# Kernel optimization log

Measured on AMD Instinct MI355X. Metric: run time of the kernel, lower is better.

## Reference

```python
import jax, jax.numpy as jnp
import numpy as np

INPUT_DIM = 512
HIDDEN_DIM = 1024


def glorot_normal(key, shape):
    fan_in, fan_out = shape[0], shape[1]
    std = jnp.sqrt(2.0 / (fan_in + fan_out))
    return std * jax.random.normal(key, shape, dtype=jnp.float32)


def setup_inputs() -> dict:
    key = jax.random.key(0)
    k1, k2, k3 = jax.random.split(key, 3)
    b, t = 32, 1024
    H = HIDDEN_DIM + INPUT_DIM
    x_btd = jax.random.normal(k1, (b, t, INPUT_DIM), dtype=jnp.float32)
    input_paddings = jnp.zeros((b, t), dtype=jnp.float32)
    kernel = glorot_normal(k2, (H, 4 * HIDDEN_DIM))  # [H, 4h]
    bias = jnp.zeros((4 * HIDDEN_DIM,), dtype=jnp.float32)
    h_init = glorot_normal(k3, (1, HIDDEN_DIM))
    return {"x_btd": x_btd, "input_paddings": input_paddings,
            "kernel": kernel, "bias": bias, "h_init": h_init}


def lstm_step(carry, x_bd, kernel, bias):
    h_bh, c_bh = carry
    x_bH = jnp.concatenate([x_bd, h_bh], axis=-1)          # [b, d+h]
    gate_out = jnp.einsum('bH,Hh->bh', x_bH, kernel) + bias  # [b, 4h]
    f, i, o, g = jnp.split(gate_out, 4, axis=-1)
    c_new = jax.nn.sigmoid(f) * c_bh + jax.nn.sigmoid(i) * jnp.tanh(g)
    h_new = jax.nn.sigmoid(o) * jnp.tanh(c_new)
    return (h_new, c_new), h_new


def reference(x_btd, input_paddings, kernel, bias, h_init) -> jnp.ndarray:
    del input_paddings
    b = x_btd.shape[0]
    h0 = jnp.tile(h_init, (b, 1))                # [b, h]
    c0 = jnp.zeros((b, HIDDEN_DIM), dtype=x_btd.dtype)
    x_tbd = jnp.transpose(x_btd, (1, 0, 2))      # [t, b, d]

    def step(carry, x_bd):
        return lstm_step(carry, x_bd, kernel, bias)

    _, h_tbh = jax.lax.scan(step, (h0, c0), x_tbd)
    return jnp.transpose(h_tbh, (1, 0, 2))       # [b, t, h]
```

## Files before the change

kernel.cpp:

```cpp
#include <hip/hip_runtime.h>


#define T_STEPS 1024
#define BATCH   32
#define DIN     512
#define HID     1024
#define KTOT    1536
#define NBLK    128
#define WCOLS   32
#define WSTR    1544
#define REDSTR  33
#define REDW    (32*REDSTR)

#define LDS_W_BYTES   (WCOLS*WSTR*2)
#define LDS_RED_BYTES (4*REDW*4)
#define LDS_H_BYTES   (256*2)
#define LDS_TOTAL     (LDS_W_BYTES + LDS_RED_BYTES + LDS_H_BYTES)

typedef __attribute__((ext_vector_type(8))) short  short8;
typedef __attribute__((ext_vector_type(4))) float  floatx4;
typedef __attribute__((ext_vector_type(4))) unsigned short ushort4_;

__device__ __forceinline__ unsigned short f2bf(float f) {
    unsigned u = __builtin_bit_cast(unsigned, f);
    u += 0x7FFFu + ((u >> 16) & 1u);
    return (unsigned short)(u >> 16);
}
__device__ __forceinline__ float sigf(float x) { return 1.f / (1.f + __expf(-x)); }

__device__ __forceinline__ floatx4 coh_load16(const void* p) {
    floatx4 v;
    asm volatile("global_load_dwordx4 %0, %1, off sc1" : "=v"(v) : "v"(p));
    return v;
}
__device__ __forceinline__ int coh_load4(const void* p) {
    int v;
    asm volatile("global_load_dword %0, %1, off sc1\n\ts_waitcnt vmcnt(0)"
                 : "=v"(v) : "v"(p) : "memory");
    return v;
}
__device__ __forceinline__ void coh_store16(void* p, short8 v) {
    asm volatile("global_store_dwordx4 %0, %1, off sc1" :: "v"(p), "v"(v) : "memory");
}
__device__ __forceinline__ void coh_store4(void* p, int v) {
    asm volatile("global_store_dword %0, %1, off sc1" :: "v"(p), "v"(v) : "memory");
}
__device__ __forceinline__ void wait_vm0() {
    asm volatile("s_waitcnt vmcnt(0)" ::: "memory");
}

__global__ __launch_bounds__(256) void prep_wt(const float* __restrict__ kern,
                                               unsigned short* __restrict__ wt) {
    __shared__ unsigned short tile[64][72];
    const int c0 = (blockIdx.x & 63) * 64;
    const int k0 = (blockIdx.x >> 6) * 64;
    const int cl = threadIdx.x & 63;
    const int kg = threadIdx.x >> 6;
    #pragma unroll
    for (int i = 0; i < 16; ++i) {
        int kl = kg * 16 + i;
        tile[cl][kl] = f2bf(kern[(k0 + kl) * 4096 + c0 + cl]);
    }
    __syncthreads();
    #pragma unroll
    for (int i = 0; i < 16; ++i) {
        int cc = kg * 16 + i;
        wt[(size_t)(c0 + cc) * KTOT + k0 + cl] = tile[cc][cl];
    }
}

__global__ __launch_bounds__(256) void prep_x(const float* __restrict__ x,
                                              unsigned short* __restrict__ xT) {
    const int row = blockIdx.x * 2 + (threadIdx.x >> 7);
    const int l   = threadIdx.x & 127;
    const int b = row >> 10, t = row & 1023;
    float4 v = ((const float4*)(x + (size_t)row * DIN))[l];
    ushort4_ o;
    o.x = f2bf(v.x); o.y = f2bf(v.y); o.z = f2bf(v.z); o.w = f2bf(v.w);
    *(ushort4_*)(xT + ((size_t)t * BATCH + b) * DIN + l * 4) = o;
}

__global__ __launch_bounds__(256) void init_h(const float* __restrict__ h_init,
                                              unsigned short* __restrict__ hbuf,
                                              int* __restrict__ flags) {
    if (blockIdx.x == 32) {
        for (int i = threadIdx.x; i < NBLK * 4; i += 256) flags[i] = 0;
        return;
    }
    const int b = blockIdx.x;
    for (int u = threadIdx.x; u < HID; u += 256)
        hbuf[b * HID + u] = f2bf(h_init[u]);
}

__global__ __launch_bounds__(256, 1) void lstm_persist(
    const unsigned short* __restrict__ wt,
    const unsigned short* __restrict__ xT,
    unsigned short* __restrict__ hbuf,
    int* __restrict__ flags,
    const float* __restrict__ bias,
    float* __restrict__ out)
{
    extern __shared__ char smem[];
    unsigned short* ldsW = (unsigned short*)smem;
    float* red = (float*)(smem + LDS_W_BYTES);
    unsigned short* hLDS = (unsigned short*)(smem + LDS_W_BYTES + LDS_RED_BYTES);

    const int bk   = blockIdx.x;
    const int tid  = threadIdx.x;
    const int wave = tid >> 6;
    const int lane = tid & 63;
    const int lrow = lane & 15;
    const int kq   = lane >> 4;

    for (int cl = wave; cl < WCOLS; cl += 4) {
        const int gcol = (cl >> 3) * HID + bk * 8 + (cl & 7);
        const unsigned short* src = wt + (size_t)gcol * KTOT;
        unsigned short* dst = ldsW + cl * WSTR;
        for (int k = lane * 8; k < KTOT; k += 512)
            *(short8*)(dst + k) = *(const short8*)(src + k);
    }

    const int pb = tid >> 3;
    const int pu = tid & 7;
    float bias_r[4];
    #pragma unroll
    for (int g = 0; g < 4; ++g) bias_r[g] = bias[g * HID + bk * 8 + pu];
    float c_state = 0.f;

    const int* myflag = flags + (wave * 32 + (lane & 31)) * 4;
    __syncthreads();

    for (int t = 0; t < T_STEPS; ++t) {
        floatx4 zero = {0.f, 0.f, 0.f, 0.f};
        floatx4 acc[2][2];
        acc[0][0] = zero; acc[0][1] = zero; acc[1][0] = zero; acc[1][1] = zero;

        const unsigned short* xb = xT + (size_t)t * (BATCH * DIN);
        #pragma unroll
        for (int i = 0; i < 4; ++i) {
            const int kl = wave * 128 + i * 32 + kq * 8;
            short8 a0 = *(const short8*)(xb + lrow * DIN + kl);
            short8 a1 = *(const short8*)(xb + (lrow + 16) * DIN + kl);
            short8 b0 = *(const short8*)(ldsW + lrow * WSTR + kl);
            short8 b1 = *(const short8*)(ldsW + (lrow + 16) * WSTR + kl);
            acc[0][0] = __builtin_amdgcn_mfma_f32_16x16x32_bf16(a0, b0, acc[0][0], 0, 0, 0);
            acc[0][1] = __builtin_amdgcn_mfma_f32_16x16x32_bf16(a0, b1, acc[0][1], 0, 0, 0);
            acc[1][0] = __builtin_amdgcn_mfma_f32_16x16x32_bf16(a1, b0, acc[1][0], 0, 0, 0);
            acc[1][1] = __builtin_amdgcn_mfma_f32_16x16x32_bf16(a1, b1, acc[1][1], 0, 0, 0);
        }

        if (t > 0) {
            while (coh_load4(myflag) < t)
                __builtin_amdgcn_s_sleep(1);
        }

        const unsigned short* hb = hbuf + (size_t)(t & 1) * (BATCH * HID);
        floatx4 ha[8][2];
        #pragma unroll
        for (int i = 0; i < 8; ++i) {
            const int kh = wave * 256 + i * 32 + kq * 8;
            ha[i][0] = coh_load16(hb + lrow * HID + kh);
            ha[i][1] = coh_load16(hb + (lrow + 16) * HID + kh);
        }
        wait_vm0();
        #pragma unroll
        for (int i = 0; i < 8; ++i) {
            const int kw = 512 + wave * 256 + i * 32 + kq * 8;
            short8 a0 = __builtin_bit_cast(short8, ha[i][0]);
            short8 a1 = __builtin_bit_cast(short8, ha[i][1]);
            short8 b0 = *(const short8*)(ldsW + lrow * WSTR + kw);
            short8 b1 = *(const short8*)(ldsW + (lrow + 16) * WSTR + kw);
            acc[0][0] = __builtin_amdgcn_mfma_f32_16x16x32_bf16(a0, b0, acc[0][0], 0, 0, 0);
            acc[0][1] = __builtin_amdgcn_mfma_f32_16x16x32_bf16(a0, b1, acc[0][1], 0, 0, 0);
            acc[1][0] = __builtin_amdgcn_mfma_f32_16x16x32_bf16(a1, b0, acc[1][0], 0, 0, 0);
            acc[1][1] = __builtin_amdgcn_mfma_f32_16x16x32_bf16(a1, b1, acc[1][1], 0, 0, 0);
        }

        #pragma unroll
        for (int mt = 0; mt < 2; ++mt)
            #pragma unroll
            for (int nt = 0; nt < 2; ++nt)
                #pragma unroll
                for (int r = 0; r < 4; ++r) {
                    const int row = mt * 16 + kq * 4 + r;
                    const int col = nt * 16 + lrow;
                    red[wave * REDW + row * REDSTR + col] = acc[mt][nt][r];
                }
        __syncthreads();

        float gv[4];
        #pragma unroll
        for (int g = 0; g < 4; ++g) {
            const int col = g * 8 + pu;
            float s = bias_r[g];
            #pragma unroll
            for (int w = 0; w < 4; ++w) s += red[w * REDW + pb * REDSTR + col];
            gv[g] = s;
        }
        const float fg = sigf(gv[0]);
        const float ig = sigf(gv[1]);
        const float og = sigf(gv[2]);
        const float gg = tanhf(gv[3]);
        c_state = fg * c_state + ig * gg;
        const float hn = og * tanhf(c_state);

        out[(size_t)pb * (T_STEPS * HID) + (size_t)t * HID + bk * 8 + pu] = hn;
        hLDS[tid] = f2bf(hn);
        __syncthreads();

        if (wave == 0) {
            if (lane < 32) {
                short8 v = *(const short8*)(hLDS + lane * 8);
                unsigned short* hp = hbuf + (size_t)((t + 1) & 1) * (BATCH * HID)
                                          + lane * HID + bk * 8;
                coh_store16(hp, v);
            }
            wait_vm0();
            if (lane == 0)
                coh_store4(flags + bk * 4, t + 1);
        }
    }
}

extern "C" void kernel_launch(void* const* d_in, const int* in_sizes, int n_in,
                              void* d_out, int out_size, void* d_ws, size_t ws_size,
                              hipStream_t stream) {
    (void)in_sizes; (void)n_in; (void)out_size;
    const float* x      = (const float*)d_in[0];
    const float* kern   = (const float*)d_in[2];
    const float* bias   = (const float*)d_in[3];
    const float* h_init = (const float*)d_in[4];
    float* out = (float*)d_out;

    char* ws = (char*)d_ws;
    unsigned short* wt    = (unsigned short*)(ws);
    unsigned short* xT    = (unsigned short*)(ws + 12582912);
    unsigned short* hbuf  = (unsigned short*)(ws + 12582912 + 33554432);
    int*            flags = (int*)(ws + 12582912 + 33554432 + 131072);
    (void)ws_size;

    hipFuncSetAttribute((const void*)lstm_persist,
                        hipFuncAttributeMaxDynamicSharedMemorySize, LDS_TOTAL);

    prep_wt<<<dim3(64 * 24), dim3(256), 0, stream>>>(kern, wt);
    prep_x<<<dim3(BATCH * T_STEPS / 2), dim3(256), 0, stream>>>(x, xT);
    init_h<<<dim3(33), dim3(256), 0, stream>>>(h_init, hbuf, flags);

    void* args[] = { &wt, &xT, &hbuf, &flags, &bias, &out };
    hipLaunchCooperativeKernel((const void*)lstm_persist, dim3(NBLK), dim3(256),
                               args, LDS_TOTAL, stream);
}
```

Before: 4.970 ms.

## Split persistent LSTM block into x-projection and recurrent-h wave groups

Doubles the block to 512 threads. Four waves compute the input projection for the next step, and the other four poll flags and compute the recurrent h contribution, so the x GEMM leaves the critical path. The h buffer is reorganised into per-producer contiguous 256-element chunks, and flags are padded to separate 64-byte lines. A fast exp-based tanh replaces tanhf, and the reduction buffer grows to 8 slots. The risks are more LDS and register pressure, a changed barrier structure, and extra __syncthreads per step.

```diff
diff --git a/kernel.cpp b/kernel.cpp
--- a/kernel.cpp
+++ b/kernel.cpp
@@ -11,9 +11,11 @@
 #define WSTR    1544
 #define REDSTR  33
 #define REDW    (32*REDSTR)
+#define NSLOT   8
+#define FLAGSTR 16
 
 #define LDS_W_BYTES   (WCOLS*WSTR*2)
-#define LDS_RED_BYTES (4*REDW*4)
+#define LDS_RED_BYTES (NSLOT*REDW*4)
 #define LDS_H_BYTES   (256*2)
 #define LDS_TOTAL     (LDS_W_BYTES + LDS_RED_BYTES + LDS_H_BYTES)
 
@@ -27,6 +29,10 @@
     return (unsigned short)(u >> 16);
 }
 __device__ __forceinline__ float sigf(float x) { return 1.f / (1.f + __expf(-x)); }
+__device__ __forceinline__ float tanh_fast(float x) {
+    float e = __expf(2.f * x);
+    return 1.f - 2.f / (e + 1.f);
+}
 
 __device__ __forceinline__ floatx4 coh_load16(const void* p) {
     floatx4 v;
@@ -84,15 +90,19 @@
                                               unsigned short* __restrict__ hbuf,
                                               int* __restrict__ flags) {
     if (blockIdx.x == 32) {
-        for (int i = threadIdx.x; i < NBLK * 4; i += 256) flags[i] = 0;
+        for (int i = threadIdx.x; i < NBLK * FLAGSTR; i += 256) flags[i] = 0;
         return;
     }
-    const int b = blockIdx.x;
-    for (int u = threadIdx.x; u < HID; u += 256)
-        hbuf[b * HID + u] = f2bf(h_init[u]);
-}
-
-__global__ __launch_bounds__(256, 1) void lstm_persist(
+    const int p0 = blockIdx.x * 4;
+    const int u = threadIdx.x & 7;
+    #pragma unroll
+    for (int j = 0; j < 4; ++j) {
+        const int p = p0 + j;
+        hbuf[p * 256 + threadIdx.x] = f2bf(h_init[p * 8 + u]);
+    }
+}
+
+__global__ __launch_bounds__(512, 2) void lstm_persist(
     const unsigned short* __restrict__ wt,
     const unsigned short* __restrict__ xT,
     unsigned short* __restrict__ hbuf,
@@ -111,8 +121,10 @@
     const int lane = tid & 63;
     const int lrow = lane & 15;
     const int kq   = lane >> 4;
-
-    for (int cl = wave; cl < WCOLS; cl += 4) {
+    const bool isG = wave < 4;
+    const int  sl  = wave & 3;
+
+    for (int cl = wave; cl < WCOLS; cl += 8) {
         const int gcol = (cl >> 3) * HID + bk * 8 + (cl & 7);
         const unsigned short* src = wt + (size_t)gcol * KTOT;
         unsigned short* dst = ldsW + cl * WSTR;
@@ -123,102 +135,167 @@
     const int pb = tid >> 3;
     const int pu = tid & 7;
     float bias_r[4];
-    #pragma unroll
-    for (int g = 0; g < 4; ++g) bias_r[g] = bias[g * HID + bk * 8 + pu];
     float c_state = 0.f;
-
-    const int* myflag = flags + (wave * 32 + (lane & 31)) * 4;
+    if (tid < 256) {
+        #pragma unroll
+        for (int g = 0; g < 4; ++g) bias_r[g] = bias[g * HID + bk * 8 + pu];
+    }
+
+    const int* myflag = flags + (sl * 32 + (lane & 31)) * FLAGSTR;
     __syncthreads();
 
-    for (int t = 0; t < T_STEPS; ++t) {
+    {
         floatx4 zero = {0.f, 0.f, 0.f, 0.f};
         floatx4 acc[2][2];
         acc[0][0] = zero; acc[0][1] = zero; acc[1][0] = zero; acc[1][1] = zero;
-
-        const unsigned short* xb = xT + (size_t)t * (BATCH * DIN);
-        #pragma unroll
-        for (int i = 0; i < 4; ++i) {
-            const int kl = wave * 128 + i * 32 + kq * 8;
-            short8 a0 = *(const short8*)(xb + lrow * DIN + kl);
-            short8 a1 = *(const short8*)(xb + (lrow + 16) * DIN + kl);
-            short8 b0 = *(const short8*)(ldsW + lrow * WSTR + kl);
-            short8 b1 = *(const short8*)(ldsW + (lrow + 16) * WSTR + kl);
-            acc[0][0] = __builtin_amdgcn_mfma_f32_16x16x32_bf16(a0, b0, acc[0][0], 0, 0, 0);
-            acc[0][1] = __builtin_amdgcn_mfma_f32_16x16x32_bf16(a0, b1, acc[0][1], 0, 0, 0);
-            acc[1][0] = __builtin_amdgcn_mfma_f32_16x16x32_bf16(a1, b0, acc[1][0], 0, 0, 0);
-            acc[1][1] = __builtin_amdgcn_mfma_f32_16x16x32_bf16(a1, b1, acc[1][1], 0, 0, 0);
+        if (isG) {
+            const unsigned short* xb = xT;
+            #pragma unroll
+            for (int i = 0; i < 4; ++i) {
+                const int kl = sl * 128 + i * 32 + kq * 8;
+                short8 a0 = *(const short8*)(xb + lrow * DIN + kl);
+                short8 a1 = *(const short8*)(xb + (lrow + 16) * DIN + kl);
+                short8 b0 = *(const short8*)(ldsW + lrow * WSTR + kl);
+                short8 b1 = *(const short8*)(ldsW + (lrow + 16) * WSTR + kl);
+                acc[0][0] = __builtin_amdgcn_mfma_f32_16x16x32_bf16(a0, b0, acc[0][0], 0, 0, 0);
+                acc[0][1] = __builtin_amdgcn_mfma_f32_16x16x32_bf16(a0, b1, acc[0][1], 0, 0, 0);
+                acc[1][0] = __builtin_amdgcn_mfma_f32_16x16x32_bf16(a1, b0, acc[1][0], 0, 0, 0);
+                acc[1][1] = __builtin_amdgcn_mfma_f32_16x16x32_bf16(a1, b1, acc[1][1], 0, 0, 0);
+            }
+        } else {
+            floatx4 ha[8][2];
+            #pragma unroll
+            for (int i = 0; i < 8; ++i) {
+                const int p = sl * 32 + i * 4 + kq;
+                ha[i][0] = coh_load16(hbuf + p * 256 + lrow * 8);
+                ha[i][1] = coh_load16(hbuf + p * 256 + (lrow + 16) * 8);
+            }
+            wait_vm0();
+            __builtin_amdgcn_sched_barrier(0);
+            #pragma unroll
+            for (int i = 0; i < 8; ++i) {
+                const int kw = 512 + sl * 256 + i * 32 + kq * 8;
+                short8 a0 = __builtin_bit_cast(short8, ha[i][0]);
+                short8 a1 = __builtin_bit_cast(short8, ha[i][1]);
+                short8 b0 = *(const short8*)(ldsW + lrow * WSTR + kw);
+                short8 b1 = *(const short8*)(ldsW + (lrow + 16) * WSTR + kw);
+                acc[0][0] = __builtin_amdgcn_mfma_f32_16x16x32_bf16(a0, b0, acc[0][0], 0, 0, 0);
+                acc[0][1] = __builtin_amdgcn_mfma_f32_16x16x32_bf16(a0, b1, acc[0][1], 0, 0, 0);
+                acc[1][0] = __builtin_amdgcn_mfma_f32_16x16x32_bf16(a1, b0, acc[1][0], 0, 0, 0);
+                acc[1][1] = __builtin_amdgcn_mfma_f32_16x16x32_bf16(a1, b1, acc[1][1], 0, 0, 0);
+            }
         }
-
-        if (t > 0) {
-            while (coh_load4(myflag) < t)
-                __builtin_amdgcn_s_sleep(1);
-        }
-
-        const unsigned short* hb = hbuf + (size_t)(t & 1) * (BATCH * HID);
-        floatx4 ha[8][2];
-        #pragma unroll
-        for (int i = 0; i < 8; ++i) {
-            const int kh = wave * 256 + i * 32 + kq * 8;
-            ha[i][0] = coh_load16(hb + lrow * HID + kh);
-            ha[i][1] = coh_load16(hb + (lrow + 16) * HID + kh);
-        }
-        wait_vm0();
-        #pragma unroll
-        for (int i = 0; i < 8; ++i) {
-            const int kw = 512 + wave * 256 + i * 32 + kq * 8;
-            short8 a0 = __builtin_bit_cast(short8, ha[i][0]);
-            short8 a1 = __builtin_bit_cast(short8, ha[i][1]);
-            short8 b0 = *(const short8*)(ldsW + lrow * WSTR + kw);
-            short8 b1 = *(const short8*)(ldsW + (lrow + 16) * WSTR + kw);
-            acc[0][0] = __builtin_amdgcn_mfma_f32_16x16x32_bf16(a0, b0, acc[0][0], 0, 0, 0);
-            acc[0][1] = __builtin_amdgcn_mfma_f32_16x16x32_bf16(a0, b1, acc[0][1], 0, 0, 0);
-            acc[1][0] = __builtin_amdgcn_mfma_f32_16x16x32_bf16(a1, b0, acc[1][0], 0, 0, 0);
-            acc[1][1] = __builtin_amdgcn_mfma_f32_16x16x32_bf16(a1, b1, acc[1][1], 0, 0, 0);
-        }
-
         #pragma unroll
         for (int mt = 0; mt < 2; ++mt)
             #pragma unroll
             for (int nt = 0; nt < 2; ++nt)
                 #pragma unroll
-                for (int r = 0; r < 4; ++r) {
-                    const int row = mt * 16 + kq * 4 + r;
-                    const int col = nt * 16 + lrow;
-                    red[wave * REDW + row * REDSTR + col] = acc[mt][nt][r];
+                for (int r = 0; r < 4; ++r)
+                    red[wave * REDW + (mt * 16 + kq * 4 + r) * REDSTR + (nt * 16 + lrow)]
+                        = acc[mt][nt][r];
+    }
+
+    for (int t = 0; t < T_STEPS; ++t) {
+        __syncthreads();
+
+        floatx4 xa[4][2];
+        if (isG && t + 1 < T_STEPS) {
+            const unsigned short* xb = xT + (size_t)(t + 1) * (BATCH * DIN);
+            #pragma unroll
+            for (int i = 0; i < 4; ++i) {
+                const int kl = sl * 128 + i * 32 + kq * 8;
+                xa[i][0] = *(const floatx4*)(xb + lrow * DIN + kl);
+                xa[i][1] = *(const floatx4*)(xb + (lrow + 16) * DIN + kl);
+            }
+        }
+
+        float gv[4];
+        if (tid < 256) {
+            #pragma unroll
+            for (int g = 0; g < 4; ++g) {
+                const int col = g * 8 + pu;
+                float s = bias_r[g];
+                #pragma unroll
+                for (int w = 0; w < NSLOT; ++w) s += red[w * REDW + pb * REDSTR + col];
+                gv[g] = s;
+            }
+            const float fg = sigf(gv[0]);
+            const float ig = sigf(gv[1]);
+            const float og = sigf(gv[2]);
+            const float gg = tanh_fast(gv[3]);
+            c_state = fg * c_state + ig * gg;
+            const float hn = og * tanh_fast(c_state);
+            out[(size_t)pb * (T_STEPS * HID) + (size_t)t * HID + bk * 8 + pu] = hn;
+            hLDS[tid] = f2bf(hn);
+        }
+        if (t == T_STEPS - 1) break;
+
+        __syncthreads();
+
+        floatx4 zero = {0.f, 0.f, 0.f, 0.f};
+        floatx4 acc[2][2];
+        acc[0][0] = zero; acc[0][1] = zero; acc[1][0] = zero; acc[1][1] = zero;
+
+        if (isG) {
+            if (wave == 0) {
+                if (lane < 32) {
+                    short8 v = *(const short8*)(hLDS + lane * 8);
+                    unsigned short* hp = hbuf + (size_t)((t + 1) & 1) * (NBLK * 256)
+                                              + bk * 256 + lane * 8;
+                    coh_store16(hp, v);
                 }
-        __syncthreads();
-
-        float gv[4];
+                wait_vm0();
+                if (lane == 0)
+                    coh_store4(flags + bk * FLAGSTR, t + 1);
+            }
+            #pragma unroll
+            for (int i = 0; i < 4; ++i) {
+                const int kl = sl * 128 + i * 32 + kq * 8;
+                short8 a0 = __builtin_bit_cast(short8, xa[i][0]);
+                short8 a1 = __builtin_bit_cast(short8, xa[i][1]);
+                short8 b0 = *(const short8*)(ldsW + lrow * WSTR + kl);
+                short8 b1 = *(const short8*)(ldsW + (lrow + 16) * WSTR + kl);
+                acc[0][0] = __builtin_amdgcn_mfma_f32_16x16x32_bf16(a0, b0, acc[0][0], 0, 0, 0);
+                acc[0][1] = __builtin_amdgcn_mfma_f32_16x16x32_bf16(a0, b1, acc[0][1], 0, 0, 0);
+                acc[1][0] = __builtin_amdgcn_mfma_f32_16x16x32_bf16(a1, b0, acc[1][0], 0, 0, 0);
+                acc[1][1] = __builtin_amdgcn_mfma_f32_16x16x32_bf16(a1, b1, acc[1][1], 0, 0, 0);
+            }
+        } else {
+            const int tgt = t + 1;
+            while (coh_load4(myflag) < tgt)
+                __builtin_amdgcn_s_sleep(1);
+            const unsigned short* hb = hbuf + (size_t)((t + 1) & 1) * (NBLK * 256);
+            floatx4 ha[8][2];
+            #pragma unroll
+            for (int i = 0; i < 8; ++i) {
+                const int p = sl * 32 + i * 4 + kq;
+                ha[i][0] = coh_load16(hb + p * 256 + lrow * 8);
+                ha[i][1] = coh_load16(hb + p * 256 + (lrow + 16) * 8);
+            }
+            wait_vm0();
+            __builtin_amdgcn_sched_barrier(0);
+            #pragma unroll
+            for (int i = 0; i < 8; ++i) {
+                const int kw = 512 + sl * 256 + i * 32 + kq * 8;
+                short8 a0 = __builtin_bit_cast(short8, ha[i][0]);
+                short8 a1 = __builtin_bit_cast(short8, ha[i][1]);
+                short8 b0 = *(const short8*)(ldsW + lrow * WSTR + kw);
+                short8 b1 = *(const short8*)(ldsW + (lrow + 16) * WSTR + kw);
+                acc[0][0] = __builtin_amdgcn_mfma_f32_16x16x32_bf16(a0, b0, acc[0][0], 0, 0, 0);
+                acc[0][1] = __builtin_amdgcn_mfma_f32_16x16x32_bf16(a0, b1, acc[0][1], 0, 0, 0);
+                acc[1][0] = __builtin_amdgcn_mfma_f32_16x16x32_bf16(a1, b0, acc[1][0], 0, 0, 0);
+                acc[1][1] = __builtin_amdgcn_mfma_f32_16x16x32_bf16(a1, b1, acc[1][1], 0, 0, 0);
+            }
+        }
+
         #pragma unroll
-        for (int g = 0; g < 4; ++g) {
-            const int col = g * 8 + pu;
-            float s = bias_r[g];
-            #pragma unroll
-            for (int w = 0; w < 4; ++w) s += red[w * REDW + pb * REDSTR + col];
-            gv[g] = s;
-        }
-        const float fg = sigf(gv[0]);
-        const float ig = sigf(gv[1]);
-        const float og = sigf(gv[2]);
-        const float gg = tanhf(gv[3]);
-        c_state = fg * c_state + ig * gg;
-        const float hn = og * tanhf(c_state);
-
-        out[(size_t)pb * (T_STEPS * HID) + (size_t)t * HID + bk * 8 + pu] = hn;
-        hLDS[tid] = f2bf(hn);
-        __syncthreads();
-
-        if (wave == 0) {
-            if (lane < 32) {
-                short8 v = *(const short8*)(hLDS + lane * 8);
-                unsigned short* hp = hbuf + (size_t)((t + 1) & 1) * (BATCH * HID)
-                                          + lane * HID + bk * 8;
-                coh_store16(hp, v);
-            }
-            wait_vm0();
-            if (lane == 0)
-                coh_store4(flags + bk * 4, t + 1);
-        }
+        for (int mt = 0; mt < 2; ++mt)
+            #pragma unroll
+            for (int nt = 0; nt < 2; ++nt)
+                #pragma unroll
+                for (int r = 0; r < 4; ++r)
+                    red[wave * REDW + (mt * 16 + kq * 4 + r) * REDSTR + (nt * 16 + lrow)]
+                        = acc[mt][nt][r];
     }
 }
 
@@ -247,6 +324,6 @@
     init_h<<<dim3(33), dim3(256), 0, stream>>>(h_init, hbuf, flags);
 
     void* args[] = { &wt, &xT, &hbuf, &flags, &bias, &out };
-    hipLaunchCooperativeKernel((const void*)lstm_persist, dim3(NBLK), dim3(256),
+    hipLaunchCooperativeKernel((const void*)lstm_persist, dim3(NBLK), dim3(512),
                                args, LDS_TOTAL, stream);
 }
```

Measured after the change: 4.356 ms. 12.4% less time.
